# Optimization experiments

Measured on AMD Instinct MI355X. Metric: run time of the kernel, lower is better.

## Reference

```python
import jax, jax.numpy as jnp
import numpy as np

B, S, D, H, HD, F = 2, 2048, 1024, 16, 64, 4096
EPS = 1e-5


def layer_norm(x, g, b):
    m = jnp.mean(x, axis=-1, keepdims=True)
    v = jnp.var(x, axis=-1, keepdims=True)
    return (x - m) * jax.lax.rsqrt(v + EPS) * g + b


def setup_inputs() -> dict:
    key = jax.random.key(0)
    ks = jax.random.split(key, 8)
    hidden_states = jax.random.normal(ks[0], (B, S, D), dtype=jnp.float32)
    # additive causal mask: 0 where allowed, -1e9 where masked
    causal = jnp.tril(jnp.ones((S, S), dtype=bool))
    attention_mask = jnp.where(causal, 0.0, -1e9).astype(jnp.float32)[None, None]
    sd = 1.0 / np.sqrt(D)
    Wq = jax.random.normal(ks[1], (D, D), jnp.float32) * sd
    Wk = jax.random.normal(ks[2], (D, D), jnp.float32) * sd
    Wv = jax.random.normal(ks[3], (D, D), jnp.float32) * sd
    Wo = jax.random.normal(ks[4], (D, D), jnp.float32) * sd
    W1 = jax.random.normal(ks[5], (D, F), jnp.float32) * sd
    W2 = jax.random.normal(ks[6], (F, D), jnp.float32) * (1.0 / np.sqrt(F))
    ln1_g = jnp.ones((D,), jnp.float32)
    ln1_b = jnp.zeros((D,), jnp.float32)
    ln2_g = jnp.ones((D,), jnp.float32)
    ln2_b = jnp.zeros((D,), jnp.float32)
    return dict(hidden_states=hidden_states, attention_mask=attention_mask,
                ln1_g=ln1_g, ln1_b=ln1_b, Wq=Wq, Wk=Wk, Wv=Wv, Wo=Wo,
                ln2_g=ln2_g, ln2_b=ln2_b, W1=W1, W2=W2)


def reference(hidden_states, attention_mask, ln1_g, ln1_b, Wq, Wk, Wv, Wo,
              ln2_g, ln2_b, W1, W2):
    x = hidden_states
    # --- attention sublayer (pre-LN) ---
    h = layer_norm(x, ln1_g, ln1_b)
    q = (h @ Wq).reshape(B, S, H, HD).transpose(0, 2, 1, 3)  # b h s d
    k = (h @ Wk).reshape(B, S, H, HD).transpose(0, 2, 1, 3)
    v = (h @ Wv).reshape(B, S, H, HD).transpose(0, 2, 1, 3)
    scores = jnp.einsum('bhqd,bhkd->bhqk', q, k) / np.sqrt(HD)
    scores = scores + attention_mask
    attn = jax.nn.softmax(scores, axis=-1)
    ctx = jnp.einsum('bhqk,bhkd->bhqd', attn, v)
    ctx = ctx.transpose(0, 2, 1, 3).reshape(B, S, D)
    x = x + ctx @ Wo
    # --- FFN sublayer (pre-LN) ---
    h = layer_norm(x, ln2_g, ln2_b)
    h = jax.nn.gelu(h @ W1, approximate=False) @ W2
    out = x + h
    return out, k, v
```

## Files before the change

kernel.cpp:

```cpp
#include <hip/hip_runtime.h>
#include <hip/hip_bf16.h>
#include <cstdint>
#include <cstddef>

#define BB 2
#define SS 2048
#define DD 1024
#define HH 16
#define HDIM 64
#define FF 4096
#define RR (BB*SS)

typedef __attribute__((ext_vector_type(8))) short short8;
typedef __attribute__((ext_vector_type(4))) float floatx4;

__device__ __forceinline__ unsigned short f2bf(float f){
    __hip_bfloat16 h = __float2bfloat16(f);
    return *reinterpret_cast<unsigned short*>(&h);
}

__device__ __forceinline__ void load_lds16(const void* g, void* l){
    __builtin_amdgcn_global_load_lds((__attribute__((address_space(1))) void*)g,
                                     (__attribute__((address_space(3))) void*)l, 16, 0, 0);
}


template<int BN, int EPI>
__global__ __launch_bounds__(256) void gemm_bt(const unsigned short* __restrict__ A,
                                               const unsigned short* __restrict__ B,
                                               int M, int N, int K, int KS,
                                               float* __restrict__ cf,
                                               const float* __restrict__ resid,
                                               unsigned short* __restrict__ cbf,
                                               unsigned short* __restrict__ qb,
                                               float* __restrict__ kout,
                                               unsigned short* __restrict__ kbf,
                                               float* __restrict__ vout)
{
    constexpr int MI_M = (BN==128) ? 4 : 2;
    __shared__ __align__(16) unsigned short As[2][128*64];
    __shared__ __align__(16) unsigned short Bs[2][BN*64];
    const int tid  = threadIdx.x;
    const int lane = tid & 63;
    const int wave = tid >> 6;
    const int quad = lane >> 4, l15 = lane & 15;
    const int wrow = (BN==128) ? (wave>>1)*64 : wave*32;
    const int wcol = (BN==128) ? (wave&1)*64 : 0;
    const int gm0 = blockIdx.y * 128, gn0 = blockIdx.x * BN;
    const int k0 = blockIdx.z * KS;
    const int niter = KS >> 6;
    const int phase = (int)((blockIdx.x + blockIdx.y) % (unsigned)niter);

    floatx4 acc[MI_M][4];
#pragma unroll
    for (int i=0;i<MI_M;i++)
#pragma unroll
        for (int j=0;j<4;j++) acc[i][j] = (floatx4){0.f,0.f,0.f,0.f};

    const int rsub = lane >> 3;
    const int d8   = (lane & 7) * 8;
    const int ksub = ((lane & 7) ^ rsub) * 8;
    constexpr int nchw = (128 + BN) / 32;

    auto stage = [&](int kt, int buf){
#pragma unroll
        for (int i=0;i<nchw;i++){
            int c = wave*nchw + i;
            if (c < 16)
                load_lds16(A + (size_t)(gm0 + c*8 + rsub)*K + kt + ksub,
                           &As[buf][c*512 + rsub*64 + d8]);
            else
                load_lds16(B + (size_t)(gn0 + (c-16)*8 + rsub)*K + kt + ksub,
                           &Bs[buf][(c-16)*512 + rsub*64 + d8]);
        }
    };

    stage(k0 + phase*64, 0);
    int cur = 0;
    for (int it=0; it<niter; it++){
        __syncthreads();
        if (it+1 < niter){
            int j = it + 1 + phase; if (j >= niter) j -= niter;
            stage(k0 + j*64, cur^1);
        }
        const unsigned short* as = As[cur];
        const unsigned short* bs = Bs[cur];
#pragma unroll
        for (int kk=0; kk<64; kk+=32){
            const int cb4 = kk >> 3;
            short8 af[MI_M], bfr[4];
#pragma unroll
            for (int mi=0;mi<MI_M;mi++){
                int row = wrow + mi*16 + l15;
                af[mi] = *(const short8*)&as[row*64 + (((cb4+quad) ^ (row&7)))*8];
            }
#pragma unroll
            for (int ni=0;ni<4;ni++){
                int row = wcol + ni*16 + l15;
                bfr[ni] = *(const short8*)&bs[row*64 + (((cb4+quad) ^ (row&7)))*8];
            }
#pragma unroll
            for (int mi=0;mi<MI_M;mi++)
#pragma unroll
                for (int ni=0;ni<4;ni++)
                    acc[mi][ni] = __builtin_amdgcn_mfma_f32_16x16x32_bf16(af[mi], bfr[ni], acc[mi][ni], 0, 0, 0);
        }
        cur ^= 1;
    }

#pragma unroll
    for (int mi=0;mi<MI_M;mi++)
#pragma unroll
        for (int ni=0;ni<4;ni++)
#pragma unroll
            for (int r=0;r<4;r++){
                int row = gm0 + wrow + mi*16 + quad*4 + r;
                int col = gn0 + wcol + ni*16 + l15;
                float v = acc[mi][ni][r];
                if constexpr (EPI == 1){
                    int region = gn0 >> 10;
                    if (region == 0){
                        qb[(size_t)row*1024 + col] = f2bf(v);
                    } else {
                        int c1 = col & 1023;
                        int h = c1 >> 6, d = c1 & 63;
                        int b = row >> 11, s = row & (SS-1);
                        size_t o = ((size_t)((b*HH + h)*SS + s))*HDIM + d;
                        if (region == 1){ kout[o] = v; kbf[o] = f2bf(v); }
                        else            { vout[o] = v; }
                    }
                } else if constexpr (EPI == 2){
                    size_t o = (size_t)row*N + col;
                    cf[o] = v + resid[o];
                } else if constexpr (EPI == 3){
                    float u = v*(0.79788456f + 0.0356774081f*v*v);
                    float g = v / (1.f + exp2f(-2.88539008f*u));
                    cbf[(size_t)row*N + col] = f2bf(g);
                } else {
                    cf[(size_t)blockIdx.z*M*N + (size_t)row*N + col] = v;
                }
            }
}

__global__ __launch_bounds__(256) void combine2_kernel(const float* __restrict__ p0,
                                                       const float* __restrict__ p1,
                                                       const float* __restrict__ resid,
                                                       float* __restrict__ out, int n4)
{
    const int i = blockIdx.x*256 + threadIdx.x;
    if (i >= n4) return;
    float4 a = ((const float4*)p0)[i];
    float4 b = ((const float4*)p1)[i];
    float4 c = ((const float4*)resid)[i];
    ((float4*)out)[i] = make_float4(a.x+b.x+c.x, a.y+b.y+c.y, a.z+b.z+c.z, a.w+b.w+c.w);
}

__global__ __launch_bounds__(256) void attn_kernel(const unsigned short* __restrict__ qbf,
                                                   const unsigned short* __restrict__ kbf,
                                                   const unsigned short* __restrict__ vtbf,
                                                   unsigned short* __restrict__ ctx)
{
    __shared__ unsigned short Ks[2][64*64];
    __shared__ unsigned short Vs[2][64*64];
    __shared__ unsigned short Ps[4][16*64];
    const int tid  = threadIdx.x;
    const int lane = tid & 63;
    const int wave = tid >> 6;
    const int quad = lane >> 4, l15 = lane & 15;
    const int aqt = blockIdx.x;
    const int bqt = 31 - aqt;
    const int bh = blockIdx.y;
    const int b = bh >> 4, h = bh & 15;
    const int q0a = aqt * 64, q0b = bqt * 64;

    const unsigned short* kb  = kbf  + (size_t)bh * SS * HDIM;
    const unsigned short* vtb = vtbf + (size_t)bh * HDIM * SS;

    const unsigned short* qra = qbf + (size_t)(b*SS + q0a + wave*16 + l15)*DD + h*HDIM + quad*8;
    const unsigned short* qrb = qbf + (size_t)(b*SS + q0b + wave*16 + l15)*DD + h*HDIM + quad*8;
    short8 qa0 = *(const short8*)qra;
    short8 qa1 = *(const short8*)(qra + 32);
    short8 qb0 = *(const short8*)qrb;
    short8 qb1 = *(const short8*)(qrb + 32);

    float lpA[4] = {0.f,0.f,0.f,0.f}, lpB[4] = {0.f,0.f,0.f,0.f};
    floatx4 accA[4], accB[4];
#pragma unroll
    for (int n=0;n<4;n++){ accA[n] = (floatx4){0.f,0.f,0.f,0.f}; accB[n] = (floatx4){0.f,0.f,0.f,0.f}; }

    const int r8 = lane >> 3;
    const int c8 = ((lane & 7) ^ r8) * 8;
    const int d8 = (lane & 7) * 8;
    const int nkt = bqt + 1;
    const float SC = 0.125f * 1.44269504f;

#pragma unroll
    for (int p=0;p<2;p++){
        int row = p*32 + wave*8 + r8;
        load_lds16(kb  + (size_t)row*HDIM + c8,  &Ks[0][row*64 + d8]);
        load_lds16(vtb + (size_t)row*SS   + c8,  &Vs[0][row*64 + d8]);
    }

    unsigned short* pl = Ps[wave];
    int cur = 0;
    for (int kt=0; kt<nkt; kt++){
        __syncthreads();
        if (kt+1 < nkt){
            int nb = cur ^ 1;
#pragma unroll
            for (int p=0;p<2;p++){
                int row = p*32 + wave*8 + r8;
                load_lds16(kb  + (size_t)((kt+1)*64 + row)*HDIM + c8, &Ks[nb][row*64 + d8]);
                load_lds16(vtb + (size_t)row*SS + (size_t)(kt+1)*64 + c8, &Vs[nb][row*64 + d8]);
            }
        }
        const unsigned short* ks = Ks[cur];
        const unsigned short* vs = Vs[cur];

        short8 kf0[4], kf1[4];
#pragma unroll
        for (int j=0;j<4;j++){
            int row = j*16 + l15;
            kf0[j] = *(const short8*)&ks[row*64 + ((quad     ^ (row&7)))*8];
            kf1[j] = *(const short8*)&ks[row*64 + (((quad+4) ^ (row&7)))*8];
        }
        short8 vf0[4], vf1[4];
#pragma unroll
        for (int n=0;n<4;n++){
            int row = n*16 + l15;
            vf0[n] = *(const short8*)&vs[row*64 + ((quad     ^ (row&7)))*8];
            vf1[n] = *(const short8*)&vs[row*64 + (((quad+4) ^ (row&7)))*8];
        }

        {
            floatx4 s[4];
#pragma unroll
            for (int j=0;j<4;j++){
                floatx4 z = (floatx4){0.f,0.f,0.f,0.f};
                z = __builtin_amdgcn_mfma_f32_16x16x32_bf16(qb0, kf0[j], z, 0, 0, 0);
                z = __builtin_amdgcn_mfma_f32_16x16x32_bf16(qb1, kf1[j], z, 0, 0, 0);
                s[j] = z;
            }
#pragma unroll
            for (int j=0;j<4;j++)
#pragma unroll
                for (int r=0;r<4;r++){
                    int prow = quad*4 + r;
                    float p = exp2f(s[j][r]*SC);
                    if (kt == bqt){
                        int row = q0b + wave*16 + prow;
                        int col = kt*64 + j*16 + l15;
                        if (col > row) p = 0.f;
                    }
                    lpB[r] += p;
                    int ch = (2*j + (l15>>3)) ^ (prow&7);
                    pl[prow*64 + ch*8 + (l15&7)] = f2bf(p);
                }
            short8 pf0 = *(const short8*)&pl[l15*64 + ((quad     ^ (l15&7)))*8];
            short8 pf1 = *(const short8*)&pl[l15*64 + (((quad+4) ^ (l15&7)))*8];
#pragma unroll
            for (int n=0;n<4;n++){
                accB[n] = __builtin_amdgcn_mfma_f32_16x16x32_bf16(pf0, vf0[n], accB[n], 0, 0, 0);
                accB[n] = __builtin_amdgcn_mfma_f32_16x16x32_bf16(pf1, vf1[n], accB[n], 0, 0, 0);
            }
        }

        if (kt <= aqt){
            floatx4 s[4];
#pragma unroll
            for (int j=0;j<4;j++){
                floatx4 z = (floatx4){0.f,0.f,0.f,0.f};
                z = __builtin_amdgcn_mfma_f32_16x16x32_bf16(qa0, kf0[j], z, 0, 0, 0);
                z = __builtin_amdgcn_mfma_f32_16x16x32_bf16(qa1, kf1[j], z, 0, 0, 0);
                s[j] = z;
            }
#pragma unroll
            for (int j=0;j<4;j++)
#pragma unroll
                for (int r=0;r<4;r++){
                    int prow = quad*4 + r;
                    float p = exp2f(s[j][r]*SC);
                    if (kt == aqt){
                        int row = q0a + wave*16 + prow;
                        int col = kt*64 + j*16 + l15;
                        if (col > row) p = 0.f;
                    }
                    lpA[r] += p;
                    int ch = (2*j + (l15>>3)) ^ (prow&7);
                    pl[prow*64 + ch*8 + (l15&7)] = f2bf(p);
                }
            short8 pf0 = *(const short8*)&pl[l15*64 + ((quad     ^ (l15&7)))*8];
            short8 pf1 = *(const short8*)&pl[l15*64 + (((quad+4) ^ (l15&7)))*8];
#pragma unroll
            for (int n=0;n<4;n++){
                accA[n] = __builtin_amdgcn_mfma_f32_16x16x32_bf16(pf0, vf0[n], accA[n], 0, 0, 0);
                accA[n] = __builtin_amdgcn_mfma_f32_16x16x32_bf16(pf1, vf1[n], accA[n], 0, 0, 0);
            }
        }
        cur ^= 1;
    }

#pragma unroll
    for (int r=0;r<4;r++){
        float va = lpA[r], vb = lpB[r];
        va += __shfl_xor(va, 1); vb += __shfl_xor(vb, 1);
        va += __shfl_xor(va, 2); vb += __shfl_xor(vb, 2);
        va += __shfl_xor(va, 4); vb += __shfl_xor(vb, 4);
        va += __shfl_xor(va, 8); vb += __shfl_xor(vb, 8);
        lpA[r] = va; lpB[r] = vb;
    }
#pragma unroll
    for (int n=0;n<4;n++)
#pragma unroll
        for (int r=0;r<4;r++){
            float oa = accA[n][r] / lpA[r];
            float ob = accB[n][r] / lpB[r];
            ctx[(size_t)(b*SS + q0a + wave*16 + quad*4 + r)*DD + h*HDIM + n*16 + l15] = f2bf(oa);
            ctx[(size_t)(b*SS + q0b + wave*16 + quad*4 + r)*DD + h*HDIM + n*16 + l15] = f2bf(ob);
        }
}

__global__ __launch_bounds__(256) void ln_kernel(const float* __restrict__ x,
                                                 const float* __restrict__ g,
                                                 const float* __restrict__ bparm,
                                                 unsigned short* __restrict__ out)
{
    __shared__ float red[8];
    const int row = blockIdx.x;
    const int tid = threadIdx.x;
    const float* xr = x + (size_t)row*DD;
    float4 v = *(const float4*)(xr + tid*4);
    float s  = v.x+v.y+v.z+v.w;
    float sq = v.x*v.x + v.y*v.y + v.z*v.z + v.w*v.w;
#pragma unroll
    for (int off=1; off<64; off<<=1){ s += __shfl_xor(s, off); sq += __shfl_xor(sq, off); }
    if ((tid & 63) == 0){ red[tid>>6] = s; red[4 + (tid>>6)] = sq; }
    __syncthreads();
    float ts = red[0]+red[1]+red[2]+red[3];
    float tq = red[4]+red[5]+red[6]+red[7];
    float mean = ts * (1.f/DD);
    float var  = tq * (1.f/DD) - mean*mean;
    float inv  = rsqrtf(var + 1e-5f);
    float4 gv = *(const float4*)(g + tid*4);
    float4 bv = *(const float4*)(bparm + tid*4);
    ushort4 o;
    o.x = f2bf((v.x-mean)*inv*gv.x + bv.x);
    o.y = f2bf((v.y-mean)*inv*gv.y + bv.y);
    o.z = f2bf((v.z-mean)*inv*gv.z + bv.z);
    o.w = f2bf((v.w-mean)*inv*gv.w + bv.w);
    *(ushort4*)(out + (size_t)row*DD + tid*4) = o;
}

__global__ __launch_bounds__(256) void castT_kernel(const float* __restrict__ in,
                                                    unsigned short* __restrict__ out,
                                                    int R, int C)
{
    __shared__ float t[32][33];
    const size_t zoff = (size_t)blockIdx.z * R * C;
    in  += zoff; out += zoff;
    const int tr = blockIdx.y*32, tc = blockIdx.x*32;
    const int lr = threadIdx.x >> 5, lc = threadIdx.x & 31;
#pragma unroll
    for (int i=0;i<4;i++)
        t[lr + i*8][lc] = in[(size_t)(tr + lr + i*8)*C + tc + lc];
    __syncthreads();
#pragma unroll
    for (int i=0;i<4;i++)
        out[(size_t)(tc + lr + i*8)*R + tr + lc] = f2bf(t[lc][lr + i*8]);
}

__global__ __launch_bounds__(256) void castT4_kernel(const float* __restrict__ i0,
                                                     const float* __restrict__ i1,
                                                     const float* __restrict__ i2,
                                                     const float* __restrict__ i3,
                                                     unsigned short* __restrict__ o0,
                                                     unsigned short* __restrict__ o1,
                                                     unsigned short* __restrict__ o2,
                                                     unsigned short* __restrict__ o3)
{
    __shared__ float t[32][33];
    const int z = blockIdx.z;
    const float* in = (z==0) ? i0 : (z==1) ? i1 : (z==2) ? i2 : i3;
    unsigned short* out = (z==0) ? o0 : (z==1) ? o1 : (z==2) ? o2 : o3;
    const int tr = blockIdx.y*32, tc = blockIdx.x*32;
    const int lr = threadIdx.x >> 5, lc = threadIdx.x & 31;
#pragma unroll
    for (int i=0;i<4;i++)
        t[lr + i*8][lc] = in[(size_t)(tr + lr + i*8)*1024 + tc + lc];
    __syncthreads();
#pragma unroll
    for (int i=0;i<4;i++)
        out[(size_t)(tc + lr + i*8)*1024 + tr + lc] = f2bf(t[lc][lr + i*8]);
}

extern "C" void kernel_launch(void* const* d_in, const int* in_sizes, int n_in,
                              void* d_out, int out_size, void* d_ws, size_t ws_size,
                              hipStream_t stream)
{
    const float* x     = (const float*)d_in[0];
    const float* ln1_g = (const float*)d_in[2];
    const float* ln1_b = (const float*)d_in[3];
    const float* Wq    = (const float*)d_in[4];
    const float* Wk    = (const float*)d_in[5];
    const float* Wv    = (const float*)d_in[6];
    const float* Wo    = (const float*)d_in[7];
    const float* ln2_g = (const float*)d_in[8];
    const float* ln2_b = (const float*)d_in[9];
    const float* W1    = (const float*)d_in[10];
    const float* W2    = (const float*)d_in[11];

    float* out  = (float*)d_out;
    float* kout = out  + (size_t)RR*DD;
    float* vout = kout + (size_t)BB*HH*SS*HDIM;

    char* w = (char*)d_ws;
    auto alloc = [&](size_t bytes) -> char* {
        char* p = w; w += (bytes + 255) & ~(size_t)255; return p;
    };
    unsigned short* qkvT  = (unsigned short*)alloc((size_t)3072*1024*2);
    unsigned short* WoT   = (unsigned short*)alloc((size_t)1024*1024*2);
    unsigned short* W1T   = (unsigned short*)alloc((size_t)4096*1024*2);
    unsigned short* W2T   = (unsigned short*)alloc((size_t)1024*4096*2);
    unsigned short* h_bf  = (unsigned short*)alloc((size_t)RR*DD*2);
    unsigned short* q_bf  = (unsigned short*)alloc((size_t)RR*DD*2);
    unsigned short* k_bf  = (unsigned short*)alloc((size_t)RR*DD*2);
    unsigned short* vt_bf = (unsigned short*)alloc((size_t)RR*DD*2);
    unsigned short* ctx_bf= (unsigned short*)alloc((size_t)RR*DD*2);
    unsigned short* act_bf= (unsigned short*)alloc((size_t)RR*FF*2);
    float* x1     = (float*)alloc((size_t)RR*DD*4);
    float* fpart  = (float*)alloc((size_t)2*RR*DD*4);

    castT4_kernel<<<dim3(32,32,4), 256, 0, stream>>>(
        Wq, Wk, Wv, Wo, qkvT, qkvT + 1024*1024, qkvT + 2*1024*1024, WoT);
    castT_kernel<<<dim3(128,32,1), 256, 0, stream>>>(W1, W1T, 1024, 4096);
    castT_kernel<<<dim3(32,128,1), 256, 0, stream>>>(W2, W2T, 4096, 1024);

    ln_kernel<<<RR, 256, 0, stream>>>(x, ln1_g, ln1_b, h_bf);
    gemm_bt<128,1><<<dim3(3072/128, RR/128), 256, 0, stream>>>(
        h_bf, qkvT, RR, 3072, 1024, 1024, nullptr, nullptr, nullptr, q_bf, kout, k_bf, vout);
    castT_kernel<<<dim3(2, 64, BB*HH), 256, 0, stream>>>(vout, vt_bf, SS, HDIM);
    attn_kernel<<<dim3(16, BB*HH), 256, 0, stream>>>(q_bf, k_bf, vt_bf, ctx_bf);
    gemm_bt<64,2><<<dim3(1024/64, RR/128), 256, 0, stream>>>(
        ctx_bf, WoT, RR, 1024, 1024, 1024, x1, x, nullptr, nullptr, nullptr, nullptr, nullptr);

    ln_kernel<<<RR, 256, 0, stream>>>(x1, ln2_g, ln2_b, h_bf);
    gemm_bt<128,3><<<dim3(4096/128, RR/128), 256, 0, stream>>>(
        h_bf, W1T, RR, 4096, 1024, 1024, nullptr, nullptr, act_bf, nullptr, nullptr, nullptr, nullptr);
    gemm_bt<128,4><<<dim3(1024/128, RR/128, 2), 256, 0, stream>>>(
        act_bf, W2T, RR, 1024, 4096, 2048, fpart, nullptr, nullptr, nullptr, nullptr, nullptr, nullptr);
    combine2_kernel<<<(RR*DD/4 + 255)/256, 256, 0, stream>>>(
        fpart, fpart + (size_t)RR*DD, x1, out, RR*DD/4);
}
```

Baseline: 376.7 us.

## Split attention KV loop across two blocks and drop FFN2 split-K

The attention kernel now launches two blocks per (query-tile pair, head). Each block handles every other KV tile and writes unnormalized fp32 partial context plus row sums, and a new combine kernel adds the two halves, normalizes and casts to bf16. This doubles attention parallelism from 512 blocks, at the cost of extra fp32 traffic and a kernel launch. Separately, the FFN down-projection drops split-K and its combine kernel. It now uses the 64-wide GEMM with a fused residual epilogue, trading the partial-sum traffic for fewer blocks.

```diff
diff --git a/kernel.cpp b/kernel.cpp
--- a/kernel.cpp
+++ b/kernel.cpp
@@ -142,23 +142,11 @@
             }
 }
 
-__global__ __launch_bounds__(256) void combine2_kernel(const float* __restrict__ p0,
-                                                       const float* __restrict__ p1,
-                                                       const float* __restrict__ resid,
-                                                       float* __restrict__ out, int n4)
-{
-    const int i = blockIdx.x*256 + threadIdx.x;
-    if (i >= n4) return;
-    float4 a = ((const float4*)p0)[i];
-    float4 b = ((const float4*)p1)[i];
-    float4 c = ((const float4*)resid)[i];
-    ((float4*)out)[i] = make_float4(a.x+b.x+c.x, a.y+b.y+c.y, a.z+b.z+c.z, a.w+b.w+c.w);
-}
-
 __global__ __launch_bounds__(256) void attn_kernel(const unsigned short* __restrict__ qbf,
                                                    const unsigned short* __restrict__ kbf,
                                                    const unsigned short* __restrict__ vtbf,
-                                                   unsigned short* __restrict__ ctx)
+                                                   float* __restrict__ pctx,
+                                                   float* __restrict__ plp)
 {
     __shared__ unsigned short Ks[2][64*64];
     __shared__ unsigned short Vs[2][64*64];
@@ -170,8 +158,12 @@
     const int aqt = blockIdx.x;
     const int bqt = 31 - aqt;
     const int bh = blockIdx.y;
+    const int z  = blockIdx.z;
     const int b = bh >> 4, h = bh & 15;
     const int q0a = aqt * 64, q0b = bqt * 64;
+
+    pctx += (size_t)z * RR * DD;
+    plp  += (size_t)z * BB * HH * SS;
 
     const unsigned short* kb  = kbf  + (size_t)bh * SS * HDIM;
     const unsigned short* vtb = vtbf + (size_t)bh * HDIM * SS;
@@ -194,26 +186,22 @@
     const int nkt = bqt + 1;
     const float SC = 0.125f * 1.44269504f;
 
-#pragma unroll
-    for (int p=0;p<2;p++){
-        int row = p*32 + wave*8 + r8;
-        load_lds16(kb  + (size_t)row*HDIM + c8,  &Ks[0][row*64 + d8]);
-        load_lds16(vtb + (size_t)row*SS   + c8,  &Vs[0][row*64 + d8]);
-    }
+    auto stageKV = [&](int kt, int buf){
+#pragma unroll
+        for (int p=0;p<2;p++){
+            int row = p*32 + wave*8 + r8;
+            load_lds16(kb  + (size_t)(kt*64 + row)*HDIM + c8, &Ks[buf][row*64 + d8]);
+            load_lds16(vtb + (size_t)row*SS + (size_t)kt*64 + c8, &Vs[buf][row*64 + d8]);
+        }
+    };
+
+    stageKV(z, 0);
 
     unsigned short* pl = Ps[wave];
     int cur = 0;
-    for (int kt=0; kt<nkt; kt++){
+    for (int kt = z; kt < nkt; kt += 2){
         __syncthreads();
-        if (kt+1 < nkt){
-            int nb = cur ^ 1;
-#pragma unroll
-            for (int p=0;p<2;p++){
-                int row = p*32 + wave*8 + r8;
-                load_lds16(kb  + (size_t)((kt+1)*64 + row)*HDIM + c8, &Ks[nb][row*64 + d8]);
-                load_lds16(vtb + (size_t)row*SS + (size_t)(kt+1)*64 + c8, &Vs[nb][row*64 + d8]);
-            }
-        }
+        if (kt+2 < nkt) stageKV(kt+2, cur^1);
         const unsigned short* ks = Ks[cur];
         const unsigned short* vs = Vs[cur];
 
@@ -236,10 +224,10 @@
             floatx4 s[4];
 #pragma unroll
             for (int j=0;j<4;j++){
-                floatx4 z = (floatx4){0.f,0.f,0.f,0.f};
-                z = __builtin_amdgcn_mfma_f32_16x16x32_bf16(qb0, kf0[j], z, 0, 0, 0);
-                z = __builtin_amdgcn_mfma_f32_16x16x32_bf16(qb1, kf1[j], z, 0, 0, 0);
-                s[j] = z;
+                floatx4 zz = (floatx4){0.f,0.f,0.f,0.f};
+                zz = __builtin_amdgcn_mfma_f32_16x16x32_bf16(qb0, kf0[j], zz, 0, 0, 0);
+                zz = __builtin_amdgcn_mfma_f32_16x16x32_bf16(qb1, kf1[j], zz, 0, 0, 0);
+                s[j] = zz;
             }
 #pragma unroll
             for (int j=0;j<4;j++)
@@ -269,10 +257,10 @@
             floatx4 s[4];
 #pragma unroll
             for (int j=0;j<4;j++){
-                floatx4 z = (floatx4){0.f,0.f,0.f,0.f};
-                z = __builtin_amdgcn_mfma_f32_16x16x32_bf16(qa0, kf0[j], z, 0, 0, 0);
-                z = __builtin_amdgcn_mfma_f32_16x16x32_bf16(qa1, kf1[j], z, 0, 0, 0);
-                s[j] = z;
+                floatx4 zz = (floatx4){0.f,0.f,0.f,0.f};
+                zz = __builtin_amdgcn_mfma_f32_16x16x32_bf16(qa0, kf0[j], zz, 0, 0, 0);
+                zz = __builtin_amdgcn_mfma_f32_16x16x32_bf16(qa1, kf1[j], zz, 0, 0, 0);
+                s[j] = zz;
             }
 #pragma unroll
             for (int j=0;j<4;j++)
@@ -313,11 +301,39 @@
     for (int n=0;n<4;n++)
 #pragma unroll
         for (int r=0;r<4;r++){
-            float oa = accA[n][r] / lpA[r];
-            float ob = accB[n][r] / lpB[r];
-            ctx[(size_t)(b*SS + q0a + wave*16 + quad*4 + r)*DD + h*HDIM + n*16 + l15] = f2bf(oa);
-            ctx[(size_t)(b*SS + q0b + wave*16 + quad*4 + r)*DD + h*HDIM + n*16 + l15] = f2bf(ob);
-        }
+            pctx[(size_t)(b*SS + q0a + wave*16 + quad*4 + r)*DD + h*HDIM + n*16 + l15] = accA[n][r];
+            pctx[(size_t)(b*SS + q0b + wave*16 + quad*4 + r)*DD + h*HDIM + n*16 + l15] = accB[n][r];
+        }
+    if (l15 == 0){
+#pragma unroll
+        for (int r=0;r<4;r++){
+            plp[(size_t)bh*SS + q0a + wave*16 + quad*4 + r] = lpA[r];
+            plp[(size_t)bh*SS + q0b + wave*16 + quad*4 + r] = lpB[r];
+        }
+    }
+}
+
+__global__ __launch_bounds__(256) void attn_combine(const float* __restrict__ p,
+                                                    const float* __restrict__ lp,
+                                                    unsigned short* __restrict__ ctx)
+{
+    const int i = blockIdx.x*256 + threadIdx.x;
+    const int row = i >> 8;
+    const int d4  = i & 255;
+    const int h   = d4 >> 4;
+    const int b   = row >> 11;
+    const int s   = row & (SS-1);
+    const size_t lpi = (size_t)(b*HH + h)*SS + s;
+    float l = lp[lpi] + lp[lpi + (size_t)BB*HH*SS];
+    float inv = 1.f / l;
+    float4 a = ((const float4*)p)[i];
+    float4 c = ((const float4*)(p + (size_t)RR*DD))[i];
+    ushort4 o;
+    o.x = f2bf((a.x+c.x)*inv);
+    o.y = f2bf((a.y+c.y)*inv);
+    o.z = f2bf((a.z+c.z)*inv);
+    o.w = f2bf((a.w+c.w)*inv);
+    *(ushort4*)(ctx + (size_t)i*4) = o;
 }
 
 __global__ __launch_bounds__(256) void ln_kernel(const float* __restrict__ x,
@@ -428,7 +444,8 @@
     unsigned short* ctx_bf= (unsigned short*)alloc((size_t)RR*DD*2);
     unsigned short* act_bf= (unsigned short*)alloc((size_t)RR*FF*2);
     float* x1     = (float*)alloc((size_t)RR*DD*4);
-    float* fpart  = (float*)alloc((size_t)2*RR*DD*4);
+    float* pctx   = (float*)alloc((size_t)2*RR*DD*4);
+    float* plp    = (float*)alloc((size_t)2*BB*HH*SS*4);
 
     castT4_kernel<<<dim3(32,32,4), 256, 0, stream>>>(
         Wq, Wk, Wv, Wo, qkvT, qkvT + 1024*1024, qkvT + 2*1024*1024, WoT);
@@ -439,15 +456,14 @@
     gemm_bt<128,1><<<dim3(3072/128, RR/128), 256, 0, stream>>>(
         h_bf, qkvT, RR, 3072, 1024, 1024, nullptr, nullptr, nullptr, q_bf, kout, k_bf, vout);
     castT_kernel<<<dim3(2, 64, BB*HH), 256, 0, stream>>>(vout, vt_bf, SS, HDIM);
-    attn_kernel<<<dim3(16, BB*HH), 256, 0, stream>>>(q_bf, k_bf, vt_bf, ctx_bf);
+    attn_kernel<<<dim3(16, BB*HH, 2), 256, 0, stream>>>(q_bf, k_bf, vt_bf, pctx, plp);
+    attn_combine<<<(RR*DD/4)/256, 256, 0, stream>>>(pctx, plp, ctx_bf);
     gemm_bt<64,2><<<dim3(1024/64, RR/128), 256, 0, stream>>>(
         ctx_bf, WoT, RR, 1024, 1024, 1024, x1, x, nullptr, nullptr, nullptr, nullptr, nullptr);
 
     ln_kernel<<<RR, 256, 0, stream>>>(x1, ln2_g, ln2_b, h_bf);
     gemm_bt<128,3><<<dim3(4096/128, RR/128), 256, 0, stream>>>(
         h_bf, W1T, RR, 4096, 1024, 1024, nullptr, nullptr, act_bf, nullptr, nullptr, nullptr, nullptr);
-    gemm_bt<128,4><<<dim3(1024/128, RR/128, 2), 256, 0, stream>>>(
-        act_bf, W2T, RR, 1024, 4096, 2048, fpart, nullptr, nullptr, nullptr, nullptr, nullptr, nullptr);
-    combine2_kernel<<<(RR*DD/4 + 255)/256, 256, 0, stream>>>(
-        fpart, fpart + (size_t)RR*DD, x1, out, RR*DD/4);
-}
+    gemm_bt<64,2><<<dim3(1024/64, RR/128), 256, 0, stream>>>(
+        act_bf, W2T, RR, 1024, 4096, 4096, out, x1, nullptr, nullptr, nullptr, nullptr, nullptr);
+}
```

After: 420.9 us. +11.7%, slower.

## Split paired causal query tiles into one tile per attention block

Applied to the files above, without the earlier changes.

The attention kernel no longer pairs a short and a long causal query tile in each block. Each block now handles a single 64-row query tile, the grid doubles to 32x32 blocks, and blocks are ordered longest-first. Launch bounds request 4 blocks per CU so more blocks can be resident, which should raise occupancy and parallelism on a GPU with many CUs. The cost is that K/V tiles are no longer shared between two query tiles, so LDS staging traffic roughly doubles and load balance now rests on the block scheduler.

```diff
diff --git a/kernel.cpp b/kernel.cpp
--- a/kernel.cpp
+++ b/kernel.cpp
@@ -155,10 +155,10 @@
     ((float4*)out)[i] = make_float4(a.x+b.x+c.x, a.y+b.y+c.y, a.z+b.z+c.z, a.w+b.w+c.w);
 }
 
-__global__ __launch_bounds__(256) void attn_kernel(const unsigned short* __restrict__ qbf,
-                                                   const unsigned short* __restrict__ kbf,
-                                                   const unsigned short* __restrict__ vtbf,
-                                                   unsigned short* __restrict__ ctx)
+__global__ __launch_bounds__(256, 4) void attn_kernel(const unsigned short* __restrict__ qbf,
+                                                      const unsigned short* __restrict__ kbf,
+                                                      const unsigned short* __restrict__ vtbf,
+                                                      unsigned short* __restrict__ ctx)
 {
     __shared__ unsigned short Ks[2][64*64];
     __shared__ unsigned short Vs[2][64*64];
@@ -167,53 +167,45 @@
     const int lane = tid & 63;
     const int wave = tid >> 6;
     const int quad = lane >> 4, l15 = lane & 15;
-    const int aqt = blockIdx.x;
-    const int bqt = 31 - aqt;
+    const int qt = 31 - (int)blockIdx.x;
     const int bh = blockIdx.y;
     const int b = bh >> 4, h = bh & 15;
-    const int q0a = aqt * 64, q0b = bqt * 64;
+    const int q0 = qt * 64;
 
     const unsigned short* kb  = kbf  + (size_t)bh * SS * HDIM;
     const unsigned short* vtb = vtbf + (size_t)bh * HDIM * SS;
 
-    const unsigned short* qra = qbf + (size_t)(b*SS + q0a + wave*16 + l15)*DD + h*HDIM + quad*8;
-    const unsigned short* qrb = qbf + (size_t)(b*SS + q0b + wave*16 + l15)*DD + h*HDIM + quad*8;
-    short8 qa0 = *(const short8*)qra;
-    short8 qa1 = *(const short8*)(qra + 32);
-    short8 qb0 = *(const short8*)qrb;
-    short8 qb1 = *(const short8*)(qrb + 32);
-
-    float lpA[4] = {0.f,0.f,0.f,0.f}, lpB[4] = {0.f,0.f,0.f,0.f};
-    floatx4 accA[4], accB[4];
-#pragma unroll
-    for (int n=0;n<4;n++){ accA[n] = (floatx4){0.f,0.f,0.f,0.f}; accB[n] = (floatx4){0.f,0.f,0.f,0.f}; }
+    const unsigned short* qr = qbf + (size_t)(b*SS + q0 + wave*16 + l15)*DD + h*HDIM + quad*8;
+    short8 qf0 = *(const short8*)qr;
+    short8 qf1 = *(const short8*)(qr + 32);
+
+    float lp[4] = {0.f,0.f,0.f,0.f};
+    floatx4 acc[4];
+#pragma unroll
+    for (int n=0;n<4;n++) acc[n] = (floatx4){0.f,0.f,0.f,0.f};
 
     const int r8 = lane >> 3;
     const int c8 = ((lane & 7) ^ r8) * 8;
     const int d8 = (lane & 7) * 8;
-    const int nkt = bqt + 1;
+    const int nkt = qt + 1;
     const float SC = 0.125f * 1.44269504f;
 
-#pragma unroll
-    for (int p=0;p<2;p++){
-        int row = p*32 + wave*8 + r8;
-        load_lds16(kb  + (size_t)row*HDIM + c8,  &Ks[0][row*64 + d8]);
-        load_lds16(vtb + (size_t)row*SS   + c8,  &Vs[0][row*64 + d8]);
-    }
+    auto stageKV = [&](int kt, int buf){
+#pragma unroll
+        for (int p=0;p<2;p++){
+            int row = p*32 + wave*8 + r8;
+            load_lds16(kb  + (size_t)(kt*64 + row)*HDIM + c8, &Ks[buf][row*64 + d8]);
+            load_lds16(vtb + (size_t)row*SS + (size_t)kt*64 + c8, &Vs[buf][row*64 + d8]);
+        }
+    };
+
+    stageKV(0, 0);
 
     unsigned short* pl = Ps[wave];
     int cur = 0;
-    for (int kt=0; kt<nkt; kt++){
+    for (int kt = 0; kt < nkt; kt++){
         __syncthreads();
-        if (kt+1 < nkt){
-            int nb = cur ^ 1;
-#pragma unroll
-            for (int p=0;p<2;p++){
-                int row = p*32 + wave*8 + r8;
-                load_lds16(kb  + (size_t)((kt+1)*64 + row)*HDIM + c8, &Ks[nb][row*64 + d8]);
-                load_lds16(vtb + (size_t)row*SS + (size_t)(kt+1)*64 + c8, &Vs[nb][row*64 + d8]);
-            }
-        }
+        if (kt+1 < nkt) stageKV(kt+1, cur^1);
         const unsigned short* ks = Ks[cur];
         const unsigned short* vs = Vs[cur];
 
@@ -224,6 +216,31 @@
             kf0[j] = *(const short8*)&ks[row*64 + ((quad     ^ (row&7)))*8];
             kf1[j] = *(const short8*)&ks[row*64 + (((quad+4) ^ (row&7)))*8];
         }
+        floatx4 s[4];
+#pragma unroll
+        for (int j=0;j<4;j++){
+            floatx4 z = (floatx4){0.f,0.f,0.f,0.f};
+            z = __builtin_amdgcn_mfma_f32_16x16x32_bf16(qf0, kf0[j], z, 0, 0, 0);
+            z = __builtin_amdgcn_mfma_f32_16x16x32_bf16(qf1, kf1[j], z, 0, 0, 0);
+            s[j] = z;
+        }
+
+#pragma unroll
+        for (int j=0;j<4;j++)
+#pragma unroll
+            for (int r=0;r<4;r++){
+                int prow = quad*4 + r;
+                float p = exp2f(s[j][r]*SC);
+                if (kt == qt){
+                    int row = q0 + wave*16 + prow;
+                    int col = kt*64 + j*16 + l15;
+                    if (col > row) p = 0.f;
+                }
+                lp[r] += p;
+                int ch = (2*j + (l15>>3)) ^ (prow&7);
+                pl[prow*64 + ch*8 + (l15&7)] = f2bf(p);
+            }
+
         short8 vf0[4], vf1[4];
 #pragma unroll
         for (int n=0;n<4;n++){
@@ -231,92 +248,31 @@
             vf0[n] = *(const short8*)&vs[row*64 + ((quad     ^ (row&7)))*8];
             vf1[n] = *(const short8*)&vs[row*64 + (((quad+4) ^ (row&7)))*8];
         }
-
-        {
-            floatx4 s[4];
-#pragma unroll
-            for (int j=0;j<4;j++){
-                floatx4 z = (floatx4){0.f,0.f,0.f,0.f};
-                z = __builtin_amdgcn_mfma_f32_16x16x32_bf16(qb0, kf0[j], z, 0, 0, 0);
-                z = __builtin_amdgcn_mfma_f32_16x16x32_bf16(qb1, kf1[j], z, 0, 0, 0);
-                s[j] = z;
-            }
-#pragma unroll
-            for (int j=0;j<4;j++)
-#pragma unroll
-                for (int r=0;r<4;r++){
-                    int prow = quad*4 + r;
-                    float p = exp2f(s[j][r]*SC);
-                    if (kt == bqt){
-                        int row = q0b + wave*16 + prow;
-                        int col = kt*64 + j*16 + l15;
-                        if (col > row) p = 0.f;
-                    }
-                    lpB[r] += p;
-                    int ch = (2*j + (l15>>3)) ^ (prow&7);
-                    pl[prow*64 + ch*8 + (l15&7)] = f2bf(p);
-                }
-            short8 pf0 = *(const short8*)&pl[l15*64 + ((quad     ^ (l15&7)))*8];
-            short8 pf1 = *(const short8*)&pl[l15*64 + (((quad+4) ^ (l15&7)))*8];
-#pragma unroll
-            for (int n=0;n<4;n++){
-                accB[n] = __builtin_amdgcn_mfma_f32_16x16x32_bf16(pf0, vf0[n], accB[n], 0, 0, 0);
-                accB[n] = __builtin_amdgcn_mfma_f32_16x16x32_bf16(pf1, vf1[n], accB[n], 0, 0, 0);
-            }
-        }
-
-        if (kt <= aqt){
-            floatx4 s[4];
-#pragma unroll
-            for (int j=0;j<4;j++){
-                floatx4 z = (floatx4){0.f,0.f,0.f,0.f};
-                z = __builtin_amdgcn_mfma_f32_16x16x32_bf16(qa0, kf0[j], z, 0, 0, 0);
-                z = __builtin_amdgcn_mfma_f32_16x16x32_bf16(qa1, kf1[j], z, 0, 0, 0);
-                s[j] = z;
-            }
-#pragma unroll
-            for (int j=0;j<4;j++)
-#pragma unroll
-                for (int r=0;r<4;r++){
-                    int prow = quad*4 + r;
-                    float p = exp2f(s[j][r]*SC);
-                    if (kt == aqt){
-                        int row = q0a + wave*16 + prow;
-                        int col = kt*64 + j*16 + l15;
-                        if (col > row) p = 0.f;
-                    }
-                    lpA[r] += p;
-                    int ch = (2*j + (l15>>3)) ^ (prow&7);
-                    pl[prow*64 + ch*8 + (l15&7)] = f2bf(p);
-                }
-            short8 pf0 = *(const short8*)&pl[l15*64 + ((quad     ^ (l15&7)))*8];
-            short8 pf1 = *(const short8*)&pl[l15*64 + (((quad+4) ^ (l15&7)))*8];
-#pragma unroll
-            for (int n=0;n<4;n++){
-                accA[n] = __builtin_amdgcn_mfma_f32_16x16x32_bf16(pf0, vf0[n], accA[n], 0, 0, 0);
-                accA[n] = __builtin_amdgcn_mfma_f32_16x16x32_bf16(pf1, vf1[n], accA[n], 0, 0, 0);
-            }
+        short8 pf0 = *(const short8*)&pl[l15*64 + ((quad     ^ (l15&7)))*8];
+        short8 pf1 = *(const short8*)&pl[l15*64 + (((quad+4) ^ (l15&7)))*8];
+#pragma unroll
+        for (int n=0;n<4;n++){
+            acc[n] = __builtin_amdgcn_mfma_f32_16x16x32_bf16(pf0, vf0[n], acc[n], 0, 0, 0);
+            acc[n] = __builtin_amdgcn_mfma_f32_16x16x32_bf16(pf1, vf1[n], acc[n], 0, 0, 0);
         }
         cur ^= 1;
     }
 
 #pragma unroll
     for (int r=0;r<4;r++){
-        float va = lpA[r], vb = lpB[r];
-        va += __shfl_xor(va, 1); vb += __shfl_xor(vb, 1);
-        va += __shfl_xor(va, 2); vb += __shfl_xor(vb, 2);
-        va += __shfl_xor(va, 4); vb += __shfl_xor(vb, 4);
-        va += __shfl_xor(va, 8); vb += __shfl_xor(vb, 8);
-        lpA[r] = va; lpB[r] = vb;
+        float v = lp[r];
+        v += __shfl_xor(v, 1);
+        v += __shfl_xor(v, 2);
+        v += __shfl_xor(v, 4);
+        v += __shfl_xor(v, 8);
+        lp[r] = v;
     }
 #pragma unroll
     for (int n=0;n<4;n++)
 #pragma unroll
         for (int r=0;r<4;r++){
-            float oa = accA[n][r] / lpA[r];
-            float ob = accB[n][r] / lpB[r];
-            ctx[(size_t)(b*SS + q0a + wave*16 + quad*4 + r)*DD + h*HDIM + n*16 + l15] = f2bf(oa);
-            ctx[(size_t)(b*SS + q0b + wave*16 + quad*4 + r)*DD + h*HDIM + n*16 + l15] = f2bf(ob);
+            float o = acc[n][r] / lp[r];
+            ctx[(size_t)(b*SS + q0 + wave*16 + quad*4 + r)*DD + h*HDIM + n*16 + l15] = f2bf(o);
         }
 }
 
@@ -439,7 +395,7 @@
     gemm_bt<128,1><<<dim3(3072/128, RR/128), 256, 0, stream>>>(
         h_bf, qkvT, RR, 3072, 1024, 1024, nullptr, nullptr, nullptr, q_bf, kout, k_bf, vout);
     castT_kernel<<<dim3(2, 64, BB*HH), 256, 0, stream>>>(vout, vt_bf, SS, HDIM);
-    attn_kernel<<<dim3(16, BB*HH), 256, 0, stream>>>(q_bf, k_bf, vt_bf, ctx_bf);
+    attn_kernel<<<dim3(32, BB*HH), 256, 0, stream>>>(q_bf, k_bf, vt_bf, ctx_bf);
     gemm_bt<64,2><<<dim3(1024/64, RR/128), 256, 0, stream>>>(
         ctx_bf, WoT, RR, 1024, 1024, 1024, x1, x, nullptr, nullptr, nullptr, nullptr, nullptr);
 
```

After: 401.8 us. 6.7% more time.
